# Kernel optimization log

Measured on AMD Instinct MI355X. Metric: run time of the kernel, lower is better.

## Reference

```python
import jax, jax.numpy as jnp
import numpy as np

D_MODEL = 1024
NHEAD = 16
HEAD_DIM = D_MODEL // NHEAD
HID = int(D_MODEL * 4.0 * (2.0 / 3.0))  # 2730, matches int(d_model*mlp_ratio*2/3)
EPS = 1e-5


def setup_inputs() -> dict:
    key = jax.random.key(0)
    ks = jax.random.split(key, 12)
    s = lambda fi, fo: (2.0 / (fi + fo)) ** 0.5
    inp = {
        "x": jax.random.normal(ks[0], (2, 2048, D_MODEL), dtype=jnp.float32),
        "ln1_w": jnp.ones((D_MODEL,), jnp.float32),
        "ln1_b": jnp.zeros((D_MODEL,), jnp.float32),
        "wq": jax.random.normal(ks[1], (D_MODEL, D_MODEL), jnp.float32) * s(D_MODEL, D_MODEL),
        "wk": jax.random.normal(ks[2], (D_MODEL, D_MODEL), jnp.float32) * s(D_MODEL, D_MODEL),
        "wv": jax.random.normal(ks[3], (D_MODEL, D_MODEL), jnp.float32) * s(D_MODEL, D_MODEL),
        "wg": jax.random.normal(ks[4], (D_MODEL, D_MODEL), jnp.float32) * s(D_MODEL, D_MODEL),
        "wo": jax.random.normal(ks[5], (D_MODEL, D_MODEL), jnp.float32) * s(D_MODEL, D_MODEL),
        "ln2_w": jnp.ones((D_MODEL,), jnp.float32),
        "ln2_b": jnp.zeros((D_MODEL,), jnp.float32),
        "w_in": jax.random.normal(ks[6], (D_MODEL, 2 * HID), jnp.float32) * s(D_MODEL, 2 * HID),
        "b_in": jnp.zeros((2 * HID,), jnp.float32),
        "w_out": jax.random.normal(ks[7], (HID, D_MODEL), jnp.float32) * s(HID, D_MODEL),
        "b_out": jnp.zeros((D_MODEL,), jnp.float32),
    }
    return inp


def _layernorm(x, w, b):
    mu = jnp.mean(x, axis=-1, keepdims=True)
    var = jnp.var(x, axis=-1, keepdims=True)
    return (x - mu) * jax.lax.rsqrt(var + EPS) * w + b


def _decay_matrix(S):
    # gamma_h = 1 - 2^{-5-h}, RetNet multiscale decays
    gamma = 1.0 - jnp.exp2(-5.0 - jnp.arange(NHEAD, dtype=jnp.float32))  # [H]
    n = jnp.arange(S, dtype=jnp.float32)
    exp = n[:, None] - n[None, :]                     # [S, S]
    mask = exp >= 0
    d = gamma[:, None, None] ** jnp.where(mask, exp, 0.0)  # [H, S, S]
    return jnp.where(mask[None], d, 0.0)


def _msr(xn, wq, wk, wv, wg, wo):
    B, S, _ = xn.shape
    split = lambda t: t.reshape(B, S, NHEAD, HEAD_DIM).transpose(0, 2, 1, 3)  # bhsd
    q = split(xn @ wq) * (HEAD_DIM ** -0.5)
    k = split(xn @ wk)
    v = split(xn @ wv)
    Dm = _decay_matrix(S)                                   # [H, S, S]
    scores = jnp.einsum("bhsd,bhtd->bhst", q, k) * Dm[None]  # causal decayed retention
    out = jnp.einsum("bhst,bhtd->bhsd", scores, v)
    # per-head normalization (GroupNorm over head dim, no affine)
    mu = jnp.mean(out, axis=-1, keepdims=True)
    var = jnp.var(out, axis=-1, keepdims=True)
    out = (out - mu) * jax.lax.rsqrt(var + 1e-6)
    out = out.transpose(0, 2, 1, 3).reshape(B, S, D_MODEL)
    out = out * jax.nn.silu(xn @ wg)                        # swish gate
    return out @ wo


def _swiglu(x, w_in, b_in, w_out, b_out):
    ab = x @ w_in + b_in
    a, b = ab[..., :HID], ab[..., HID:]
    return (a * jax.nn.silu(b)) @ w_out + b_out


def reference(x, ln1_w, ln1_b, wq, wk, wv, wg, wo, ln2_w, ln2_b, w_in, b_in, w_out, b_out):
    h = _msr(_layernorm(x, ln1_w, ln1_b), wq, wk, wv, wg, wo)
    x = x + h  # dropout/drop_path identity at eval
    x = x + _swiglu(_layernorm(x, ln2_w, ln2_b), w_in, b_in, w_out, b_out)
    return x
```

## Files before the change

### kernel.cpp

```cpp
#include <hip/hip_runtime.h>
#include <math.h>

#define D_MODEL 1024
#define NHEAD   16
#define HDIM    64
#define HID     2730
#define HID_PAD 2816
#define SEQ     2048
#define BATCH   2
#define NTOK    (BATCH * SEQ)
#define QKG     3072

typedef __attribute__((ext_vector_type(8))) short bf16x8;
typedef __attribute__((ext_vector_type(4))) float f32x4;
typedef __attribute__((ext_vector_type(4))) short s16x4;

static __device__ inline short f2bf(float f)
{
    union { float f; unsigned int u; } c; c.f = f;
    unsigned int r = c.u + 0x7FFFu + ((c.u >> 16) & 1u);
    return (short)(r >> 16);
}
static __device__ inline float bf2f(short s)
{
    union { unsigned int u; float f; } c;
    c.u = ((unsigned int)(unsigned short)s) << 16;
    return c.f;
}

#define GLD16(gsrc, ldst) \
    __builtin_amdgcn_global_load_lds((const __attribute__((address_space(1))) void*)(gsrc), \
                                     (__attribute__((address_space(3))) void*)(ldst), 16, 0, 0)


__global__ void ln_kernel(const float* __restrict__ x,
                          const float* __restrict__ w,
                          const float* __restrict__ b,
                          short* __restrict__ out,
                          float eps)
{
    int row = blockIdx.x;
    int t = threadIdx.x;
    const float4* xr = (const float4*)(x + (size_t)row * D_MODEL);
    float4 v = xr[t];
    float s  = v.x + v.y + v.z + v.w;
    float sq = v.x * v.x + v.y * v.y + v.z * v.z + v.w * v.w;
#pragma unroll
    for (int off = 32; off > 0; off >>= 1) {
        s  += __shfl_xor(s, off);
        sq += __shfl_xor(sq, off);
    }
    __shared__ float ss[4], ssq[4];
    int wave = t >> 6;
    if ((t & 63) == 0) { ss[wave] = s; ssq[wave] = sq; }
    __syncthreads();
    s  = ss[0] + ss[1] + ss[2] + ss[3];
    sq = ssq[0] + ssq[1] + ssq[2] + ssq[3];
    float mu  = s * (1.0f / D_MODEL);
    float var = sq * (1.0f / D_MODEL) - mu * mu;
    float inv = rsqrtf(var + eps);
    float4 wv = ((const float4*)w)[t];
    float4 bv = ((const float4*)b)[t];
    s16x4 o;
    o.x = f2bf((v.x - mu) * inv * wv.x + bv.x);
    o.y = f2bf((v.y - mu) * inv * wv.y + bv.y);
    o.z = f2bf((v.z - mu) * inv * wv.z + bv.z);
    o.w = f2bf((v.w - mu) * inv * wv.w + bv.w);
    *(s16x4*)(out + (size_t)row * D_MODEL + 4 * t) = o;
}

struct TJob {
    const float* src;
    short* dst;
    int ldsrc, coloff, nvalid, kvalid, KPAD, NPAD;
};
struct TJobs { TJob j[8]; };

__global__ __launch_bounds__(256) void transpose_all(TJobs jobs)
{
    TJob jb = jobs.j[blockIdx.z];
    int k0 = blockIdx.x * 64, n0 = blockIdx.y * 64;
    if (k0 >= jb.KPAD || n0 >= jb.NPAD) return;
    __shared__ float tile[64][65];
    int t = threadIdx.x;
    {
        int kk = t >> 2, np = (t & 3) << 4;
        int k = k0 + kk;
        bool kok = k < jb.kvalid;
        const float* srow = jb.src + (size_t)k * jb.ldsrc + jb.coloff + n0 + np;
#pragma unroll
        for (int i = 0; i < 16; ++i) {
            int n = n0 + np + i;
            tile[kk][np + i] = (kok && n < jb.nvalid) ? srow[i] : 0.0f;
        }
    }
    __syncthreads();
    {
        int nn = t >> 2, kp = (t & 3) << 4;
        short* drow = jb.dst + (size_t)(n0 + nn) * jb.KPAD + k0 + kp;
#pragma unroll
        for (int v4 = 0; v4 < 4; ++v4) {
            s16x4 o;
            o.x = f2bf(tile[kp + v4 * 4 + 0][nn]);
            o.y = f2bf(tile[kp + v4 * 4 + 1][nn]);
            o.z = f2bf(tile[kp + v4 * 4 + 2][nn]);
            o.w = f2bf(tile[kp + v4 * 4 + 3][nn]);
            *(s16x4*)(drow + v4 * 4) = o;
        }
    }
}

template<int EPI>
static __device__ __forceinline__ void gemm_core(
        const short* __restrict__ A, int lda,
        const short* __restrict__ Bt,
        const float* __restrict__ bias,
        const float* __restrict__ R, int ldr,
        void* __restrict__ C, int ldc, int K, int bm, int bn,
        short (*As)[4096], short (*Bs)[4096])
{
    int t = threadIdx.x;
    int w = t >> 6;
    int lane = t & 63;
    int quad = lane >> 4;
    int l15  = lane & 15;
    int x7   = l15 & 7;

    int p0 = t >> 3;
    int u  = (t & 7) ^ (p0 & 7);
    int scol = (u & 3) << 3;
    const short* gA0 = A  + (size_t)(bm + p0 + ((u >> 2) << 6)) * lda + scol;
    const short* gA1 = gA0 + (size_t)32 * lda;
    const short* gB0 = Bt + (size_t)(bn + p0 + ((u >> 2) << 6)) * K + scol;
    const short* gB1 = gB0 + (size_t)32 * K;
    int wb = w << 9;

    int wr = (w >> 1) * 64;
    int wc = (w & 1) * 64;
    int aoff = l15 * 64 + (((((w >> 1) << 2) | quad) ^ x7) << 3);
    int boff = l15 * 64 + (((((w & 1) << 2) | quad) ^ x7) << 3);

    f32x4 acc[4][4];
#pragma unroll
    for (int i = 0; i < 4; ++i)
#pragma unroll
        for (int j = 0; j < 4; ++j) acc[i][j] = (f32x4){0.f, 0.f, 0.f, 0.f};

    GLD16(gA0, &As[0][wb]);
    GLD16(gA1, &As[0][2048 + wb]);
    GLD16(gB0, &Bs[0][wb]);
    GLD16(gB1, &Bs[0][2048 + wb]);

    for (int k0 = 0; k0 < K; k0 += 32) {
        int cur = (k0 >> 5) & 1;
        __syncthreads();
        int k1 = k0 + 32;
        if (k1 < K) {
            GLD16(gA0 + k1, &As[cur ^ 1][wb]);
            GLD16(gA1 + k1, &As[cur ^ 1][2048 + wb]);
            GLD16(gB0 + k1, &Bs[cur ^ 1][wb]);
            GLD16(gB1 + k1, &Bs[cur ^ 1][2048 + wb]);
        }
        bf16x8 af[4], bfr[4];
#pragma unroll
        for (int i = 0; i < 4; ++i)
            af[i] = *(const bf16x8*)(&As[cur][i * 1024 + aoff]);
#pragma unroll
        for (int j = 0; j < 4; ++j)
            bfr[j] = *(const bf16x8*)(&Bs[cur][j * 1024 + boff]);
#pragma unroll
        for (int i = 0; i < 4; ++i)
#pragma unroll
            for (int j = 0; j < 4; ++j)
                acc[i][j] = __builtin_amdgcn_mfma_f32_16x16x32_bf16(af[i], bfr[j], acc[i][j], 0, 0, 0);
    }

#pragma unroll
    for (int i = 0; i < 4; ++i) {
        int gr = bm + wr + i * 16 + quad * 4;
#pragma unroll
        for (int j = 0; j < 4; ++j) {
            int gc = bn + wc + j * 16 + l15;
#pragma unroll
            for (int r = 0; r < 4; ++r) {
                float val = acc[i][j][r];
                size_t idx = (size_t)(gr + r) * ldc + gc;
                if (EPI == 0) {
                    ((short*)C)[idx] = f2bf(val);
                } else if (EPI == 1) {
                    ((float*)C)[idx] = val + R[(size_t)(gr + r) * ldr + gc];
                } else {
                    ((float*)C)[idx] = val + bias[gc] + R[(size_t)(gr + r) * ldr + gc];
                }
            }
        }
    }
}

__global__ __launch_bounds__(256, 4) void proj_kernel(
        const short* __restrict__ xn,
        const short* __restrict__ qkgT,
        short* __restrict__ qkg,
        const short* __restrict__ wvT,
        short* __restrict__ vT)
{
    __shared__ short As[2][4096];
    __shared__ short Bs[2][4096];
    int id = blockIdx.x;
    if (id < 768) {
        int bm = (id & 31) * 128, bn = (id >> 5) * 128;
        gemm_core<0>(xn, D_MODEL, qkgT, nullptr, nullptr, 0, qkg, QKG, D_MODEL, bm, bn, As, Bs);
    } else {
        int i2 = id - 768;
        int bn = (i2 & 31) * 128, bm = (i2 >> 5) * 128;
        gemm_core<0>(wvT, D_MODEL, xn, nullptr, nullptr, 0, vT, NTOK, D_MODEL, bm, bn, As, Bs);
    }
}

template<int EPI>
__global__ __launch_bounds__(256, 4) void gemm_n64(
        const short* __restrict__ A, int lda,
        const short* __restrict__ Bt,
        const float* __restrict__ bias,
        const float* __restrict__ R, int ldr,
        void* __restrict__ C, int ldc, int K)
{
    __shared__ short As[2][4096];
    __shared__ short Bs[2][2048];
    int bm = blockIdx.x * 128;
    int bn = blockIdx.y * 64;
    int t = threadIdx.x;
    int w = t >> 6;
    int lane = t & 63;
    int quad = lane >> 4;
    int l15  = lane & 15;
    int x7   = l15 & 7;

    int p0 = t >> 3;
    int u  = (t & 7) ^ (p0 & 7);
    int scol = (u & 3) << 3;
    const short* gA0 = A  + (size_t)(bm + p0 + ((u >> 2) << 6)) * lda + scol;
    const short* gA1 = gA0 + (size_t)32 * lda;
    const short* gB0 = Bt + (size_t)(bn + p0 + ((u >> 2) << 5)) * K + scol;
    int wb = w << 9;

    int wr = (w >> 1) * 64;
    int wc = (w & 1) * 32;
    int aoff = l15 * 64 + (((((w >> 1) << 2) | quad) ^ x7) << 3);
    int boff = l15 * 64 + (((((w & 1) << 2) | quad) ^ x7) << 3);

    f32x4 acc[4][2];
#pragma unroll
    for (int i = 0; i < 4; ++i)
#pragma unroll
        for (int j = 0; j < 2; ++j) acc[i][j] = (f32x4){0.f, 0.f, 0.f, 0.f};

    GLD16(gA0, &As[0][wb]);
    GLD16(gA1, &As[0][2048 + wb]);
    GLD16(gB0, &Bs[0][wb]);

    for (int k0 = 0; k0 < K; k0 += 32) {
        int cur = (k0 >> 5) & 1;
        __syncthreads();
        int k1 = k0 + 32;
        if (k1 < K) {
            GLD16(gA0 + k1, &As[cur ^ 1][wb]);
            GLD16(gA1 + k1, &As[cur ^ 1][2048 + wb]);
            GLD16(gB0 + k1, &Bs[cur ^ 1][wb]);
        }
        bf16x8 af[4], bfr[2];
#pragma unroll
        for (int i = 0; i < 4; ++i)
            af[i] = *(const bf16x8*)(&As[cur][i * 1024 + aoff]);
#pragma unroll
        for (int j = 0; j < 2; ++j)
            bfr[j] = *(const bf16x8*)(&Bs[cur][j * 1024 + boff]);
#pragma unroll
        for (int i = 0; i < 4; ++i)
#pragma unroll
            for (int j = 0; j < 2; ++j)
                acc[i][j] = __builtin_amdgcn_mfma_f32_16x16x32_bf16(af[i], bfr[j], acc[i][j], 0, 0, 0);
    }

#pragma unroll
    for (int i = 0; i < 4; ++i) {
        int gr = bm + wr + i * 16 + quad * 4;
#pragma unroll
        for (int j = 0; j < 2; ++j) {
            int gc = bn + wc + j * 16 + l15;
#pragma unroll
            for (int r = 0; r < 4; ++r) {
                float val = acc[i][j][r];
                size_t idx = (size_t)(gr + r) * ldc + gc;
                if (EPI == 0) {
                    ((short*)C)[idx] = f2bf(val);
                } else if (EPI == 1) {
                    ((float*)C)[idx] = val + R[(size_t)(gr + r) * ldr + gc];
                } else {
                    ((float*)C)[idx] = val + bias[gc] + R[(size_t)(gr + r) * ldr + gc];
                }
            }
        }
    }
}

__global__ __launch_bounds__(256, 4) void mlp_fused(
        const short* __restrict__ A,
        const short* __restrict__ w_inT,
        const float* __restrict__ b_in,
        short* __restrict__ hm)
{
    __shared__ short As[2][4096];
    __shared__ short Ba[2][2048];
    __shared__ short Bb[2][2048];
    const int K = D_MODEL;
    int bm = blockIdx.x * 128;
    int bn = blockIdx.y * 64;
    int t = threadIdx.x;
    int w = t >> 6;
    int lane = t & 63;
    int quad = lane >> 4;
    int l15  = lane & 15;
    int x7   = l15 & 7;

    int p0 = t >> 3;
    int u  = (t & 7) ^ (p0 & 7);
    int scol = (u & 3) << 3;
    const short* gA0 = A + (size_t)(bm + p0 + ((u >> 2) << 6)) * K + scol;
    const short* gA1 = gA0 + (size_t)32 * K;
    const short* gBa = w_inT + (size_t)(bn + p0 + ((u >> 2) << 5)) * K + scol;
    const short* gBb = gBa + (size_t)HID_PAD * K;
    int wb = w << 9;

    int wr = (w >> 1) * 64;
    int wc = (w & 1) * 32;
    int aoff = l15 * 64 + (((((w >> 1) << 2) | quad) ^ x7) << 3);
    int boff = l15 * 64 + (((((w & 1) << 2) | quad) ^ x7) << 3);

    f32x4 acca[4][2], accb[4][2];
#pragma unroll
    for (int i = 0; i < 4; ++i)
#pragma unroll
        for (int j = 0; j < 2; ++j) {
            acca[i][j] = (f32x4){0.f, 0.f, 0.f, 0.f};
            accb[i][j] = (f32x4){0.f, 0.f, 0.f, 0.f};
        }

    GLD16(gA0, &As[0][wb]);
    GLD16(gA1, &As[0][2048 + wb]);
    GLD16(gBa, &Ba[0][wb]);
    GLD16(gBb, &Bb[0][wb]);

    for (int k0 = 0; k0 < K; k0 += 32) {
        int cur = (k0 >> 5) & 1;
        __syncthreads();
        int k1 = k0 + 32;
        if (k1 < K) {
            GLD16(gA0 + k1, &As[cur ^ 1][wb]);
            GLD16(gA1 + k1, &As[cur ^ 1][2048 + wb]);
            GLD16(gBa + k1, &Ba[cur ^ 1][wb]);
            GLD16(gBb + k1, &Bb[cur ^ 1][wb]);
        }
        bf16x8 af[4], baf[2], bbf[2];
#pragma unroll
        for (int i = 0; i < 4; ++i)
            af[i] = *(const bf16x8*)(&As[cur][i * 1024 + aoff]);
#pragma unroll
        for (int j = 0; j < 2; ++j) {
            baf[j] = *(const bf16x8*)(&Ba[cur][j * 1024 + boff]);
            bbf[j] = *(const bf16x8*)(&Bb[cur][j * 1024 + boff]);
        }
#pragma unroll
        for (int i = 0; i < 4; ++i)
#pragma unroll
            for (int j = 0; j < 2; ++j) {
                acca[i][j] = __builtin_amdgcn_mfma_f32_16x16x32_bf16(af[i], baf[j], acca[i][j], 0, 0, 0);
                accb[i][j] = __builtin_amdgcn_mfma_f32_16x16x32_bf16(af[i], bbf[j], accb[i][j], 0, 0, 0);
            }
    }

#pragma unroll
    for (int i = 0; i < 4; ++i) {
        int gr = bm + wr + i * 16 + quad * 4;
#pragma unroll
        for (int j = 0; j < 2; ++j) {
            int gc = bn + wc + j * 16 + l15;
            bool ok = gc < HID;
            float ba = ok ? b_in[gc] : 0.0f;
            float bb = ok ? b_in[HID + gc] : 0.0f;
#pragma unroll
            for (int r = 0; r < 4; ++r) {
                float a  = acca[i][j][r] + ba;
                float bv = accb[i][j][r] + bb;
                float val = ok ? a * (bv / (1.0f + expf(-bv))) : 0.0f;
                hm[(size_t)(gr + r) * HID_PAD + gc] = f2bf(val);
            }
        }
    }
}

#define PSTR 72

__global__ __launch_bounds__(512) void retention_mfma(
        const short* __restrict__ qkg,
        const short* __restrict__ vT,
        short* __restrict__ rg)
{
    int qb = (int)gridDim.x - 1 - (int)blockIdx.x;
    int h  = blockIdx.y;
    int b  = blockIdx.z;

    __shared__ short ks[2][4096];
    __shared__ short vt[2][4096];
    __shared__ short ps[8][16 * PSTR];

    int tid  = threadIdx.x;
    int w    = tid >> 6;
    int lane = tid & 63;
    int quad = lane >> 4;
    int l15  = lane & 15;
    int x7   = l15 & 7;

    float log2g = log1pf(-exp2f(-5.0f - (float)h)) * 1.4426950408889634f;
    int hcol = h * HDIM;
    int s0 = qb * 128;
    size_t tok0 = (size_t)b * SEQ;

    int sch  = tid >> 8;
    int p0r  = (tid >> 3) & 31;
    int ur   = (tid & 7) ^ (p0r & 7);
    int srw  = p0r + ((ur >> 2) << 5);
    int sc8  = (ur & 3) << 3;
    const short* kbase  = qkg + (tok0 + srw) * QKG + 1024 + hcol + sch * 32 + sc8;
    const short* vtbase = vT + (size_t)(hcol + srw) * NTOK + tok0 + sch * 32 + sc8;
    int lb = tid << 3;

    const short* qrow = qkg + (tok0 + s0 + w * 16 + l15) * QKG + hcol;
    bf16x8 qa0 = *(const bf16x8*)(qrow + quad * 8);
    bf16x8 qa1 = *(const bf16x8*)(qrow + 32 + quad * 8);

    float colfac[4];
#pragma unroll
    for (int tile = 0; tile < 4; ++tile)
        colfac[tile] = exp2f(-(float)(tile * 16 + l15) * log2g) * 0.125f;

    f32x4 oacc[4];
#pragma unroll
    for (int i = 0; i < 4; ++i) oacc[i] = (f32x4){0.f, 0.f, 0.f, 0.f};

    int sbase = s0 + w * 16 + quad * 4;
    int tmax = 2 * qb + 1;

    GLD16(kbase, &ks[0][lb]);
    GLD16(vtbase, &vt[0][lb]);

    for (int tb = 0; tb <= tmax; ++tb) {
        int cur = tb & 1;
        __syncthreads();
        if (tb < tmax) {
            GLD16(kbase + (size_t)(tb + 1) * 64 * QKG, &ks[cur ^ 1][lb]);
            GLD16(vtbase + (tb + 1) * 64, &vt[cur ^ 1][lb]);
        }

        f32x4 sacc[4];
#pragma unroll
        for (int i = 0; i < 4; ++i) sacc[i] = (f32x4){0.f, 0.f, 0.f, 0.f};
#pragma unroll
        for (int tile = 0; tile < 4; ++tile) {
            int kaddr = ((tile & 1) * 16 + l15) * 64 +
                        (((((tile >> 1) << 2) | quad) ^ x7) << 3);
            bf16x8 kb0 = *(const bf16x8*)(&ks[cur][kaddr]);
            bf16x8 kb1 = *(const bf16x8*)(&ks[cur][2048 + kaddr]);
            sacc[tile] = __builtin_amdgcn_mfma_f32_16x16x32_bf16(qa0, kb0, sacc[tile], 0, 0, 0);
            sacc[tile] = __builtin_amdgcn_mfma_f32_16x16x32_bf16(qa1, kb1, sacc[tile], 0, 0, 0);
        }

        int fbi = sbase - tb * 64;
        float rf[4];
#pragma unroll
        for (int reg = 0; reg < 4; ++reg)
            rf[reg] = exp2f((float)(fbi + reg) * log2g);

        if (tb * 64 + 63 > s0 + w * 16) {
#pragma unroll
            for (int tile = 0; tile < 4; ++tile) {
                int tt = tile * 16 + l15;
#pragma unroll
                for (int reg = 0; reg < 4; ++reg) {
                    float p = (fbi + reg >= tt) ? sacc[tile][reg] * rf[reg] * colfac[tile] : 0.0f;
                    ps[w][(quad * 4 + reg) * PSTR + tile * 16 + l15] = f2bf(p);
                }
            }
        } else {
#pragma unroll
            for (int tile = 0; tile < 4; ++tile)
#pragma unroll
                for (int reg = 0; reg < 4; ++reg)
                    ps[w][(quad * 4 + reg) * PSTR + tile * 16 + l15] =
                        f2bf(sacc[tile][reg] * (rf[reg] * colfac[tile]));
        }

#pragma unroll
        for (int ksi = 0; ksi < 2; ++ksi) {
            bf16x8 pa = *(const bf16x8*)(&ps[w][l15 * PSTR + ksi * 32 + quad * 8]);
#pragma unroll
            for (int dt = 0; dt < 4; ++dt) {
                int vaddr = ((dt & 1) * 16 + l15) * 64 +
                            (((((dt >> 1) << 2) | quad) ^ x7) << 3);
                bf16x8 vb = *(const bf16x8*)(&vt[cur][ksi * 2048 + vaddr]);
                oacc[dt] = __builtin_amdgcn_mfma_f32_16x16x32_bf16(pa, vb, oacc[dt], 0, 0, 0);
            }
        }
    }

    float s1[4], s2[4];
#pragma unroll
    for (int reg = 0; reg < 4; ++reg) {
        s1[reg] = oacc[0][reg] + oacc[1][reg] + oacc[2][reg] + oacc[3][reg];
        s2[reg] = oacc[0][reg] * oacc[0][reg] + oacc[1][reg] * oacc[1][reg]
                + oacc[2][reg] * oacc[2][reg] + oacc[3][reg] * oacc[3][reg];
    }
#pragma unroll
    for (int off = 1; off < 16; off <<= 1) {
#pragma unroll
        for (int reg = 0; reg < 4; ++reg) {
            s1[reg] += __shfl_xor(s1[reg], off);
            s2[reg] += __shfl_xor(s2[reg], off);
        }
    }
    size_t rowtok = tok0 + s0 + w * 16 + quad * 4;
    short* obase = rg + rowtok * D_MODEL + hcol;
    const short* gbase = qkg + rowtok * QKG + 2048 + hcol;
#pragma unroll
    for (int reg = 0; reg < 4; ++reg) {
        float mu  = s1[reg] * (1.0f / 64.0f);
        float var = s2[reg] * (1.0f / 64.0f) - mu * mu;
        float inv = rsqrtf(var + 1e-6f);
#pragma unroll
        for (int dt = 0; dt < 4; ++dt) {
            float gv = bf2f(gbase[(size_t)reg * QKG + dt * 16 + l15]);
            float val = (oacc[dt][reg] - mu) * inv * (gv / (1.0f + expf(-gv)));
            obase[(size_t)reg * D_MODEL + dt * 16 + l15] = f2bf(val);
        }
    }
}

extern "C" void kernel_launch(void* const* d_in, const int* in_sizes, int n_in,
                              void* d_out, int out_size, void* d_ws, size_t ws_size,
                              hipStream_t stream)
{
    const float* x     = (const float*)d_in[0];
    const float* ln1w  = (const float*)d_in[1];
    const float* ln1b  = (const float*)d_in[2];
    const float* wq    = (const float*)d_in[3];
    const float* wk    = (const float*)d_in[4];
    const float* wv    = (const float*)d_in[5];
    const float* wg    = (const float*)d_in[6];
    const float* wo    = (const float*)d_in[7];
    const float* ln2w  = (const float*)d_in[8];
    const float* ln2b  = (const float*)d_in[9];
    const float* w_in  = (const float*)d_in[10];
    const float* b_in  = (const float*)d_in[11];
    const float* w_out = (const float*)d_in[12];
    const float* b_out = (const float*)d_in[13];
    float* out = (float*)d_out;
    char* base = (char*)d_ws;

    const size_t MB = 1u << 20;
    short* xn     = (short*)(base);
    short* qkgT   = (short*)(base +  8 * MB);
    short* wvT    = (short*)(base + 14 * MB);
    short* woT    = (short*)(base + 16 * MB);
    short* w_inT  = (short*)(base + 18 * MB);
    short* w_outT = (short*)(base + 29 * MB);
    short* qkg    = (short*)(base + 35 * MB);
    short* hm     = (short*)(base + 35 * MB);
    short* vT     = (short*)(base + 59 * MB);
    short* rg     = (short*)(base + 67 * MB);

    TJobs jobs;
    jobs.j[0] = { wq,    qkgT,                          1024,    0, 1024, 1024, 1024, 1024 };
    jobs.j[1] = { wk,    qkgT + 1024 * 1024,            1024,    0, 1024, 1024, 1024, 1024 };
    jobs.j[2] = { wg,    qkgT + 2 * 1024 * 1024,        1024,    0, 1024, 1024, 1024, 1024 };
    jobs.j[3] = { wv,    wvT,                           1024,    0, 1024, 1024, 1024, 1024 };
    jobs.j[4] = { wo,    woT,                           1024,    0, 1024, 1024, 1024, 1024 };
    jobs.j[5] = { w_in,  w_inT,                         2 * HID, 0,   HID, 1024, 1024, HID_PAD };
    jobs.j[6] = { w_in,  w_inT + (size_t)HID_PAD * 1024, 2 * HID, HID, HID, 1024, 1024, HID_PAD };
    jobs.j[7] = { w_out, w_outT,                        1024,    0, 1024, HID, HID_PAD, 1024 };
    transpose_all<<<dim3(44, 44, 8), 256, 0, stream>>>(jobs);

    ln_kernel<<<NTOK, 256, 0, stream>>>(x, ln1w, ln1b, xn, 1e-5f);
    proj_kernel<<<1024, 256, 0, stream>>>(xn, qkgT, qkg, wvT, vT);
    retention_mfma<<<dim3(SEQ / 128, NHEAD, BATCH), 512, 0, stream>>>(qkg, vT, rg);
    gemm_n64<1><<<dim3(32, 16), 256, 0, stream>>>(rg, D_MODEL, woT, nullptr, x, D_MODEL, out, D_MODEL, D_MODEL);
    ln_kernel<<<NTOK, 256, 0, stream>>>(out, ln2w, ln2b, xn, 1e-5f);
    mlp_fused<<<dim3(NTOK / 128, HID_PAD / 64), 256, 0, stream>>>(xn, w_inT, b_in, hm);
    gemm_n64<2><<<dim3(32, 16), 256, 0, stream>>>(hm, HID_PAD, w_outT, b_out, out, D_MODEL, out, D_MODEL, HID_PAD);
}
```

Baseline: 406.7 us.

## Enlarge mlp_fused tile to 256 rows with interleaved gate/value B tile

The fused SwiGLU input GEMM now computes a 256x64 output tile per block instead of 128x64, with each warp holding 8x4 MFMA accumulators. The A and B shared tiles are enlarged, and the B tile interleaves the 'a' and 'b' halves of w_in in 16-row groups so each warp's adjacent fragments pair up for the gating epilogue. This raises arithmetic intensity per shared-memory load and halves the number of blocks. The cost is higher register pressure, which is why launch bounds drop to 2 blocks per CU, plus fewer blocks in flight to hide latency.

```diff
diff --git a/kernel.cpp b/kernel.cpp
--- a/kernel.cpp
+++ b/kernel.cpp
@@ -304,17 +304,16 @@
     }
 }
 
-__global__ __launch_bounds__(256, 4) void mlp_fused(
+__global__ __launch_bounds__(256, 2) void mlp_fused(
         const short* __restrict__ A,
         const short* __restrict__ w_inT,
         const float* __restrict__ b_in,
         short* __restrict__ hm)
 {
-    __shared__ short As[2][4096];
-    __shared__ short Ba[2][2048];
-    __shared__ short Bb[2][2048];
+    __shared__ short As[2][8192];
+    __shared__ short Bs[2][4096];
     const int K = D_MODEL;
-    int bm = blockIdx.x * 128;
+    int bm = blockIdx.x * 256;
     int bn = blockIdx.y * 64;
     int t = threadIdx.x;
     int w = t >> 6;
@@ -323,75 +322,70 @@
     int l15  = lane & 15;
     int x7   = l15 & 7;
 
-    int p0 = t >> 3;
-    int u  = (t & 7) ^ (p0 & 7);
-    int scol = (u & 3) << 3;
-    const short* gA0 = A + (size_t)(bm + p0 + ((u >> 2) << 6)) * K + scol;
-    const short* gA1 = gA0 + (size_t)32 * K;
-    const short* gBa = w_inT + (size_t)(bn + p0 + ((u >> 2) << 5)) * K + scol;
-    const short* gBb = gBa + (size_t)HID_PAD * K;
-    int wb = w << 9;
-
-    int wr = (w >> 1) * 64;
-    int wc = (w & 1) * 32;
-    int aoff = l15 * 64 + (((((w >> 1) << 2) | quad) ^ x7) << 3);
-    int boff = l15 * 64 + (((((w & 1) << 2) | quad) ^ x7) << 3);
-
-    f32x4 acca[4][2], accb[4][2];
-#pragma unroll
-    for (int i = 0; i < 4; ++i)
-#pragma unroll
-        for (int j = 0; j < 2; ++j) {
-            acca[i][j] = (f32x4){0.f, 0.f, 0.f, 0.f};
-            accb[i][j] = (f32x4){0.f, 0.f, 0.f, 0.f};
-        }
-
-    GLD16(gA0, &As[0][wb]);
-    GLD16(gA1, &As[0][2048 + wb]);
-    GLD16(gBa, &Ba[0][wb]);
-    GLD16(gBb, &Bb[0][wb]);
+    int li3 = lane >> 3;
+    int u   = (lane & 7) ^ li3;
+    int hi  = u >> 2;
+    int qk  = (u & 3) << 3;
+    const short* gA = A + (size_t)(bm + hi * 128 + w * 32 + li3) * K + qk;
+    int f = hi * 4 + w;
+    const short* gB = w_inT + (size_t)(((f & 1) ? HID_PAD : 0) + bn
+                                       + ((f >> 1) << 4) + li3) * K + qk;
+
+    int abase = l15 * 64 + ((((w >> 1) << 2) | quad) ^ x7) * 8;
+    int bbase = l15 * 64 + ((((w & 1) << 2) | quad) ^ x7) * 8;
+
+    f32x4 acc[8][4];
+#pragma unroll
+    for (int i = 0; i < 8; ++i)
+#pragma unroll
+        for (int j = 0; j < 4; ++j) acc[i][j] = (f32x4){0.f, 0.f, 0.f, 0.f};
+
+#pragma unroll
+    for (int c = 0; c < 4; ++c)
+        GLD16(gA + (size_t)c * 8 * K, &As[0][w * 2048 + c * 512]);
+#pragma unroll
+    for (int c = 0; c < 2; ++c)
+        GLD16(gB + (size_t)c * 8 * K, &Bs[0][w * 1024 + c * 512]);
 
     for (int k0 = 0; k0 < K; k0 += 32) {
         int cur = (k0 >> 5) & 1;
         __syncthreads();
         int k1 = k0 + 32;
         if (k1 < K) {
-            GLD16(gA0 + k1, &As[cur ^ 1][wb]);
-            GLD16(gA1 + k1, &As[cur ^ 1][2048 + wb]);
-            GLD16(gBa + k1, &Ba[cur ^ 1][wb]);
-            GLD16(gBb + k1, &Bb[cur ^ 1][wb]);
-        }
-        bf16x8 af[4], baf[2], bbf[2];
-#pragma unroll
-        for (int i = 0; i < 4; ++i)
-            af[i] = *(const bf16x8*)(&As[cur][i * 1024 + aoff]);
-#pragma unroll
-        for (int j = 0; j < 2; ++j) {
-            baf[j] = *(const bf16x8*)(&Ba[cur][j * 1024 + boff]);
-            bbf[j] = *(const bf16x8*)(&Bb[cur][j * 1024 + boff]);
-        }
-#pragma unroll
-        for (int i = 0; i < 4; ++i)
-#pragma unroll
-            for (int j = 0; j < 2; ++j) {
-                acca[i][j] = __builtin_amdgcn_mfma_f32_16x16x32_bf16(af[i], baf[j], acca[i][j], 0, 0, 0);
-                accb[i][j] = __builtin_amdgcn_mfma_f32_16x16x32_bf16(af[i], bbf[j], accb[i][j], 0, 0, 0);
-            }
-    }
-
-#pragma unroll
-    for (int i = 0; i < 4; ++i) {
-        int gr = bm + wr + i * 16 + quad * 4;
-#pragma unroll
-        for (int j = 0; j < 2; ++j) {
-            int gc = bn + wc + j * 16 + l15;
+#pragma unroll
+            for (int c = 0; c < 4; ++c)
+                GLD16(gA + (size_t)c * 8 * K + k1, &As[cur ^ 1][w * 2048 + c * 512]);
+#pragma unroll
+            for (int c = 0; c < 2; ++c)
+                GLD16(gB + (size_t)c * 8 * K + k1, &Bs[cur ^ 1][w * 1024 + c * 512]);
+        }
+        bf16x8 af[8], bfr[4];
+#pragma unroll
+        for (int m = 0; m < 8; ++m)
+            af[m] = *(const bf16x8*)(&As[cur][m * 1024 + abase]);
+#pragma unroll
+        for (int jf = 0; jf < 4; ++jf)
+            bfr[jf] = *(const bf16x8*)(&Bs[cur][jf * 1024 + bbase]);
+#pragma unroll
+        for (int m = 0; m < 8; ++m)
+#pragma unroll
+            for (int jf = 0; jf < 4; ++jf)
+                acc[m][jf] = __builtin_amdgcn_mfma_f32_16x16x32_bf16(af[m], bfr[jf], acc[m][jf], 0, 0, 0);
+    }
+
+#pragma unroll
+    for (int m = 0; m < 8; ++m) {
+        int gr = bm + (w >> 1) * 128 + m * 16 + quad * 4;
+#pragma unroll
+        for (int jj = 0; jj < 2; ++jj) {
+            int gc = bn + (((w & 1) << 1) + jj) * 16 + l15;
             bool ok = gc < HID;
             float ba = ok ? b_in[gc] : 0.0f;
             float bb = ok ? b_in[HID + gc] : 0.0f;
 #pragma unroll
             for (int r = 0; r < 4; ++r) {
-                float a  = acca[i][j][r] + ba;
-                float bv = accb[i][j][r] + bb;
+                float a  = acc[m][2 * jj][r] + ba;
+                float bv = acc[m][2 * jj + 1][r] + bb;
                 float val = ok ? a * (bv / (1.0f + expf(-bv))) : 0.0f;
                 hm[(size_t)(gr + r) * HID_PAD + gc] = f2bf(val);
             }
@@ -594,6 +588,6 @@
     retention_mfma<<<dim3(SEQ / 128, NHEAD, BATCH), 512, 0, stream>>>(qkg, vT, rg);
     gemm_n64<1><<<dim3(32, 16), 256, 0, stream>>>(rg, D_MODEL, woT, nullptr, x, D_MODEL, out, D_MODEL, D_MODEL);
     ln_kernel<<<NTOK, 256, 0, stream>>>(out, ln2w, ln2b, xn, 1e-5f);
-    mlp_fused<<<dim3(NTOK / 128, HID_PAD / 64), 256, 0, stream>>>(xn, w_inT, b_in, hm);
+    mlp_fused<<<dim3(NTOK / 256, HID_PAD / 64), 256, 0, stream>>>(xn, w_inT, b_in, hm);
     gemm_n64<2><<<dim3(32, 16), 256, 0, stream>>>(hm, HID_PAD, w_outT, b_out, out, D_MODEL, out, D_MODEL, HID_PAD);
 }
```

Result: faster. 397.0 us (-2.4%).
